# Kernel optimization log

Hardware: AMD Instinct MI355X
Metric: run time of the kernel (lower is better)

Reference implementation:

```python
import jax, jax.numpy as jnp
import numpy as np

HEADS = 8
DIM_HEAD = 64
SCALE = DIM_HEAD ** -0.5

def setup_inputs() -> dict:
    key = jax.random.key(0)
    ks = jax.random.split(key, 6)
    b, n, m, qd, cd = 4, 2048, 2048, 256, 256
    inner = HEADS * DIM_HEAD
    return {
        "x": jax.random.normal(ks[0], (b, n, qd), jnp.float32),
        "context": jax.random.normal(ks[1], (b, m, cd), jnp.float32),
        "Wq": jax.random.normal(ks[2], (inner, qd), jnp.float32) * 0.02,
        "bq": jnp.zeros((inner,), jnp.float32),
        "Wkv": jax.random.normal(ks[3], (2 * inner, cd), jnp.float32) * 0.02,
        "bkv": jnp.zeros((2 * inner,), jnp.float32),
        "Wo": jax.random.normal(ks[4], (qd, inner), jnp.float32) * 0.02,
        "bo": jnp.zeros((qd,), jnp.float32),
    }

def reference(x, context, Wq, bq, Wkv, bkv, Wo, bo):
    b, n, _ = x.shape
    m = context.shape[1]
    inner = HEADS * DIM_HEAD
    # 1x1 conv projections == pointwise linear
    q = jnp.einsum('bnd,ed->bne', x, Wq) + bq            # [b, n, inner]
    kv = jnp.einsum('bmd,ed->bme', context, Wkv) + bkv    # [b, m, 2*inner]
    k, v = kv[..., :inner], kv[..., inner:]
    q = q.reshape(b, n, HEADS, DIM_HEAD).transpose(0, 2, 1, 3)  # [b,h,n,d]
    k = k.reshape(b, m, HEADS, DIM_HEAD).transpose(0, 2, 1, 3)
    v = v.reshape(b, m, HEADS, DIM_HEAD).transpose(0, 2, 1, 3)
    sim = jnp.einsum('bhid,bhjd->bhij', q, k) * SCALE     # [b,h,n,m]
    attn = jax.nn.softmax(sim, axis=-1)
    out = jnp.einsum('bhij,bhjd->bhid', attn, v)          # [b,h,n,d]
    out = out.transpose(0, 2, 1, 3).reshape(b, n, inner)  # [b,n,inner]
    return jnp.einsum('bne,oe->bno', out, Wo) + bo        # [b,n,query_dim]
```

## Files before the change

kernel.cpp:

```cpp
#include <hip/hip_runtime.h>
#include <hip/hip_bf16.h>

#define NB 4
#define SEQ 2048
#define NHEADS 8

typedef __attribute__((ext_vector_type(8))) short bf16x8;
typedef __attribute__((ext_vector_type(4))) short bf16x4;
typedef __attribute__((ext_vector_type(4))) float f32x4;

__device__ inline short f2bf(float x) {
    union { float f; unsigned u; } v; v.f = x;
    unsigned r = v.u + 0x7FFF + ((v.u >> 16) & 1);
    return (short)(r >> 16);
}

__device__ inline unsigned pack2bf(float a, float b) {
    __hip_bfloat162 h = __float22bfloat162_rn(make_float2(a, b));
    unsigned u; __builtin_memcpy(&u, &h, 4);
    return u;
}

__device__ inline bf16x8 pack8(float4 a, float4 b) {
    union { unsigned u[4]; bf16x8 v; } r;
    r.u[0] = pack2bf(a.x, a.y);
    r.u[1] = pack2bf(a.z, a.w);
    r.u[2] = pack2bf(b.x, b.y);
    r.u[3] = pack2bf(b.z, b.w);
    return r.v;
}

__global__ __launch_bounds__(256) void cvt_xc(
    const float* __restrict__ x, const float* __restrict__ ctx,
    short* __restrict__ xb, short* __restrict__ cb)
{
    const int i = blockIdx.x * 256 + threadIdx.x;
    const float* src; short* dst; int off;
    if (i < 524288) { src = x;   dst = xb; off = i; }
    else            { src = ctx; dst = cb; off = i - 524288; }
    const float4 v = ((const float4*)src)[off];
    uint2 o2;
    o2.x = pack2bf(v.x, v.y);
    o2.y = pack2bf(v.z, v.w);
    *(uint2*)(dst + (size_t)off * 4) = o2;
}

template <bool CVT_A, bool CVT_W, bool OUT_BF16>
__global__ __launch_bounds__(256) void gemm128(
    const void* __restrict__ A_, const void* __restrict__ W_,
    const float* __restrict__ bias, void* __restrict__ out,
    int K, int Ccols, float scale)
{
    __shared__ short As[128 * 64];
    __shared__ short Ws[128 * 64];
    const int tid = threadIdx.x;
    const int w = tid >> 6, lane = tid & 63, low = lane & 15, quad = lane >> 4;
    const int wm = w >> 1, wn = w & 1;
    const int rM0 = blockIdx.y * 128, c0 = blockIdx.x * 128;
    const int srow = tid >> 3, sj = tid & 7;

    f32x4 acc[4][4];
#pragma unroll
    for (int mt = 0; mt < 4; ++mt)
#pragma unroll
        for (int nt = 0; nt < 4; ++nt) acc[mt][nt] = (f32x4){0.f, 0.f, 0.f, 0.f};

    float4 paf[4][2], pwf[4][2];
    bf16x8 pab[4], pwb[4];

    auto loadA = [&](int c, int k0) {
        const int row = c * 32 + srow;
        if constexpr (CVT_A) {
            const float* p = (const float*)A_ + (size_t)(rM0 + row) * K + k0 + sj * 8;
            paf[c][0] = ((const float4*)p)[0];
            paf[c][1] = ((const float4*)p)[1];
        } else {
            pab[c] = *(const bf16x8*)((const short*)A_ + (size_t)(rM0 + row) * K + k0 + sj * 8);
        }
    };
    auto loadW = [&](int c, int k0) {
        const int row = c * 32 + srow;
        if constexpr (CVT_W) {
            const float* p = (const float*)W_ + (size_t)(c0 + row) * K + k0 + sj * 8;
            pwf[c][0] = ((const float4*)p)[0];
            pwf[c][1] = ((const float4*)p)[1];
        } else {
            pwb[c] = *(const bf16x8*)((const short*)W_ + (size_t)(c0 + row) * K + k0 + sj * 8);
        }
    };

#pragma unroll
    for (int c = 0; c < 4; ++c) { loadA(c, 0); loadW(c, 0); }

    int k0 = 0;
    for (;;) {
        __syncthreads();
#pragma unroll
        for (int c = 0; c < 4; ++c) {
            const int row = c * 32 + srow;
            const int pc = sj ^ (row & 7);
            if constexpr (CVT_A) *(bf16x8*)(&As[row * 64 + pc * 8]) = pack8(paf[c][0], paf[c][1]);
            else                 *(bf16x8*)(&As[row * 64 + pc * 8]) = pab[c];
            if constexpr (CVT_W) *(bf16x8*)(&Ws[row * 64 + pc * 8]) = pack8(pwf[c][0], pwf[c][1]);
            else                 *(bf16x8*)(&Ws[row * 64 + pc * 8]) = pwb[c];
        }
        __syncthreads();
        const int kn = k0 + 64;
        if (kn < K) {
#pragma unroll
            for (int c = 0; c < 4; ++c) { loadA(c, kn); loadW(c, kn); }
        }
#pragma unroll
        for (int kh = 0; kh < 2; ++kh) {
            bf16x8 af[4], bfv[4];
#pragma unroll
            for (int t = 0; t < 4; ++t) {
                const int ra = wm * 64 + t * 16 + low;
                af[t] = *(const bf16x8*)(&As[ra * 64 + ((kh * 4 + quad) ^ (ra & 7)) * 8]);
                const int rb = wn * 64 + t * 16 + low;
                bfv[t] = *(const bf16x8*)(&Ws[rb * 64 + ((kh * 4 + quad) ^ (rb & 7)) * 8]);
            }
#pragma unroll
            for (int mt = 0; mt < 4; ++mt)
#pragma unroll
                for (int nt = 0; nt < 4; ++nt)
                    acc[mt][nt] = __builtin_amdgcn_mfma_f32_16x16x32_bf16(af[mt], bfv[nt], acc[mt][nt], 0, 0, 0);
        }
        k0 = kn;
        if (k0 >= K) break;
    }

#pragma unroll
    for (int nt = 0; nt < 4; ++nt) {
        const int col = c0 + wn * 64 + nt * 16 + low;
        const float bv = bias[col];
#pragma unroll
        for (int mt = 0; mt < 4; ++mt) {
            const size_t rbase = (size_t)(rM0 + wm * 64 + mt * 16 + quad * 4);
#pragma unroll
            for (int r = 0; r < 4; ++r) {
                const float val = (acc[mt][nt][r] + bv) * scale;
                if (OUT_BF16) ((short*)out)[(rbase + r) * Ccols + col] = f2bf(val);
                else          ((float*)out)[(rbase + r) * Ccols + col] = val;
            }
        }
    }
}

template <bool CVT_A, bool CVT_W, bool OUT_BF16>
__global__ __launch_bounds__(256) void gemm64(
    const void* __restrict__ A_, const void* __restrict__ W_,
    const float* __restrict__ bias, void* __restrict__ out,
    int K, int Ccols, float scale)
{
    __shared__ short As[64 * 64];
    __shared__ short Ws[64 * 64];
    const int tid = threadIdx.x;
    const int w = tid >> 6, lane = tid & 63, low = lane & 15, quad = lane >> 4;
    const int wm = w >> 1, wn = w & 1;
    const int r0 = blockIdx.y * 64, c0 = blockIdx.x * 64;
    const int srow = tid >> 2;
    const int sc = (tid & 3) * 2;

    f32x4 acc[2][2];
#pragma unroll
    for (int mt = 0; mt < 2; ++mt)
#pragma unroll
        for (int nt = 0; nt < 2; ++nt) acc[mt][nt] = (f32x4){0.f, 0.f, 0.f, 0.f};

    float4 paf[2][2], pwf[2][2];
    bf16x8 pab[2], pwb[2];

    auto loadA = [&](int k0) {
        if constexpr (CVT_A) {
            const float* p = (const float*)A_ + (size_t)(r0 + srow) * K + k0 + sc * 8;
            paf[0][0] = ((const float4*)p)[0]; paf[0][1] = ((const float4*)p)[1];
            paf[1][0] = ((const float4*)p)[2]; paf[1][1] = ((const float4*)p)[3];
        } else {
            const short* p = (const short*)A_ + (size_t)(r0 + srow) * K + k0 + sc * 8;
            pab[0] = ((const bf16x8*)p)[0];
            pab[1] = ((const bf16x8*)p)[1];
        }
    };
    auto loadW = [&](int k0) {
        if constexpr (CVT_W) {
            const float* p = (const float*)W_ + (size_t)(c0 + srow) * K + k0 + sc * 8;
            pwf[0][0] = ((const float4*)p)[0]; pwf[0][1] = ((const float4*)p)[1];
            pwf[1][0] = ((const float4*)p)[2]; pwf[1][1] = ((const float4*)p)[3];
        } else {
            const short* p = (const short*)W_ + (size_t)(c0 + srow) * K + k0 + sc * 8;
            pwb[0] = ((const bf16x8*)p)[0];
            pwb[1] = ((const bf16x8*)p)[1];
        }
    };

    loadA(0); loadW(0);

    int k0 = 0;
    for (;;) {
        __syncthreads();
#pragma unroll
        for (int c = 0; c < 2; ++c) {
            const int pc = (sc + c) ^ (srow & 7);
            if constexpr (CVT_A) *(bf16x8*)(&As[srow * 64 + pc * 8]) = pack8(paf[c][0], paf[c][1]);
            else                 *(bf16x8*)(&As[srow * 64 + pc * 8]) = pab[c];
            if constexpr (CVT_W) *(bf16x8*)(&Ws[srow * 64 + pc * 8]) = pack8(pwf[c][0], pwf[c][1]);
            else                 *(bf16x8*)(&Ws[srow * 64 + pc * 8]) = pwb[c];
        }
        __syncthreads();
        const int kn = k0 + 64;
        if (kn < K) { loadA(kn); loadW(kn); }
#pragma unroll
        for (int kh = 0; kh < 2; ++kh) {
            bf16x8 af[2], bfv[2];
#pragma unroll
            for (int t = 0; t < 2; ++t) {
                const int ra = wm * 32 + t * 16 + low;
                af[t] = *(const bf16x8*)(&As[ra * 64 + ((kh * 4 + quad) ^ (ra & 7)) * 8]);
                const int rb = wn * 32 + t * 16 + low;
                bfv[t] = *(const bf16x8*)(&Ws[rb * 64 + ((kh * 4 + quad) ^ (rb & 7)) * 8]);
            }
#pragma unroll
            for (int mt = 0; mt < 2; ++mt)
#pragma unroll
                for (int nt = 0; nt < 2; ++nt)
                    acc[mt][nt] = __builtin_amdgcn_mfma_f32_16x16x32_bf16(af[mt], bfv[nt], acc[mt][nt], 0, 0, 0);
        }
        k0 = kn;
        if (k0 >= K) break;
    }

#pragma unroll
    for (int nt = 0; nt < 2; ++nt) {
        const int col = c0 + wn * 32 + nt * 16 + low;
        const float bv = bias[col];
#pragma unroll
        for (int mt = 0; mt < 2; ++mt) {
            const size_t rbase = (size_t)(r0 + wm * 32 + mt * 16 + quad * 4);
#pragma unroll
            for (int r = 0; r < 4; ++r) {
                const float val = (acc[mt][nt][r] + bv) * scale;
                if (OUT_BF16) ((short*)out)[(rbase + r) * Ccols + col] = f2bf(val);
                else          ((float*)out)[(rbase + r) * Ccols + col] = val;
            }
        }
    }
}

#define KST 72
#define VST 72
#define PST 72

__global__ __launch_bounds__(256) void attn_mfma(
    const short* __restrict__ q2,
    const short* __restrict__ kv2,
    short* __restrict__ o)
{
    __shared__ short Ks[64 * KST];
    __shared__ short Vt[64 * VST];
    __shared__ short Ps[4][32 * PST];

    const int tid = threadIdx.x;
    const int w = tid >> 6;
    const int lane = tid & 63;
    const int low = lane & 15;
    const int quad = lane >> 4;

    const int flat = blockIdx.x;
    const int h = flat & 7;
    const int rest = flat >> 3;
    const int qtile = rest & 15;
    const int b = rest >> 4;
    const int iq0 = qtile * 128;

    bf16x8 qf[2][2];
#pragma unroll
    for (int qt = 0; qt < 2; ++qt)
#pragma unroll
        for (int kh = 0; kh < 2; ++kh)
            qf[qt][kh] = *(const bf16x8*)(q2 + (size_t)(b * SEQ + iq0 + w * 32 + qt * 16 + low) * 512
                                          + h * 64 + kh * 32 + quad * 8);

    const short* kbase = kv2 + (size_t)(b * SEQ) * 1024 + h * 64;
    const short* vbase = kbase + 512;
    short* pw = &Ps[w][0];

    float lsum[2] = {0.f, 0.f};
    f32x4 oacc[2][4];
#pragma unroll
    for (int qt = 0; qt < 2; ++qt)
#pragma unroll
        for (int dt = 0; dt < 4; ++dt) oacc[qt][dt] = (f32x4){0.f, 0.f, 0.f, 0.f};

    const int krow = tid >> 2;
    const int kc = (tid & 3) * 16;
    const int vk4 = (tid & 15) * 4;
    const int vd4 = (tid >> 4) * 4;

    bf16x8 pk0, pk1;
    bf16x4 pv0, pv1, pv2, pv3;
    {
        const short* ksrc = kbase + (size_t)krow * 1024 + kc;
        pk0 = *(const bf16x8*)(ksrc);
        pk1 = *(const bf16x8*)(ksrc + 8);
        const short* vs = vbase + (size_t)vk4 * 1024 + vd4;
        pv0 = *(const bf16x4*)(vs);
        pv1 = *(const bf16x4*)(vs + 1024);
        pv2 = *(const bf16x4*)(vs + 2048);
        pv3 = *(const bf16x4*)(vs + 3072);
    }

    for (int jt = 0; jt < SEQ / 64; ++jt) {
        __syncthreads();
        *(bf16x8*)(&Ks[krow * KST + kc]) = pk0;
        *(bf16x8*)(&Ks[krow * KST + kc + 8]) = pk1;
        {
            bf16x4 c0_, c1_, c2_, c3_;
            c0_[0] = pv0[0]; c0_[1] = pv1[0]; c0_[2] = pv2[0]; c0_[3] = pv3[0];
            c1_[0] = pv0[1]; c1_[1] = pv1[1]; c1_[2] = pv2[1]; c1_[3] = pv3[1];
            c2_[0] = pv0[2]; c2_[1] = pv1[2]; c2_[2] = pv2[2]; c2_[3] = pv3[2];
            c3_[0] = pv0[3]; c3_[1] = pv1[3]; c3_[2] = pv2[3]; c3_[3] = pv3[3];
            *(bf16x4*)(&Vt[(vd4 + 0) * VST + vk4]) = c0_;
            *(bf16x4*)(&Vt[(vd4 + 1) * VST + vk4]) = c1_;
            *(bf16x4*)(&Vt[(vd4 + 2) * VST + vk4]) = c2_;
            *(bf16x4*)(&Vt[(vd4 + 3) * VST + vk4]) = c3_;
        }
        __syncthreads();

        if (jt + 1 < SEQ / 64) {
            const short* ksrc = kbase + (size_t)((jt + 1) * 64 + krow) * 1024 + kc;
            pk0 = *(const bf16x8*)(ksrc);
            pk1 = *(const bf16x8*)(ksrc + 8);
            const short* vs = vbase + (size_t)((jt + 1) * 64 + vk4) * 1024 + vd4;
            pv0 = *(const bf16x4*)(vs);
            pv1 = *(const bf16x4*)(vs + 1024);
            pv2 = *(const bf16x4*)(vs + 2048);
            pv3 = *(const bf16x4*)(vs + 3072);
        }

#pragma unroll
        for (int nt = 0; nt < 4; ++nt) {
            const bf16x8 kf0 = *(const bf16x8*)(&Ks[(nt * 16 + low) * KST + quad * 8]);
            const bf16x8 kf1 = *(const bf16x8*)(&Ks[(nt * 16 + low) * KST + 32 + quad * 8]);
#pragma unroll
            for (int qt = 0; qt < 2; ++qt) {
                f32x4 s = (f32x4){0.f, 0.f, 0.f, 0.f};
                s = __builtin_amdgcn_mfma_f32_16x16x32_bf16(kf0, qf[qt][0], s, 0, 0, 0);
                s = __builtin_amdgcn_mfma_f32_16x16x32_bf16(kf1, qf[qt][1], s, 0, 0, 0);
                const float p0 = __builtin_amdgcn_exp2f(s[0]);
                const float p1 = __builtin_amdgcn_exp2f(s[1]);
                const float p2 = __builtin_amdgcn_exp2f(s[2]);
                const float p3 = __builtin_amdgcn_exp2f(s[3]);
                lsum[qt] += (p0 + p1) + (p2 + p3);
                uint2 u;
                u.x = pack2bf(p0, p1);
                u.y = pack2bf(p2, p3);
                *(uint2*)(&pw[(qt * 16 + low) * PST + nt * 16 + quad * 4]) = u;
            }
        }
        __builtin_amdgcn_wave_barrier();

#pragma unroll
        for (int kb = 0; kb < 2; ++kb) {
            bf16x8 pfr[2];
#pragma unroll
            for (int qt = 0; qt < 2; ++qt)
                pfr[qt] = *(const bf16x8*)(&pw[(qt * 16 + low) * PST + kb * 32 + quad * 8]);
#pragma unroll
            for (int dt = 0; dt < 4; ++dt) {
                const bf16x8 vf = *(const bf16x8*)(&Vt[(dt * 16 + low) * VST + kb * 32 + quad * 8]);
                oacc[0][dt] = __builtin_amdgcn_mfma_f32_16x16x32_bf16(pfr[0], vf, oacc[0][dt], 0, 0, 0);
                oacc[1][dt] = __builtin_amdgcn_mfma_f32_16x16x32_bf16(pfr[1], vf, oacc[1][dt], 0, 0, 0);
            }
        }
        __builtin_amdgcn_wave_barrier();
    }

#pragma unroll
    for (int qt = 0; qt < 2; ++qt) {
        float lv = lsum[qt];
        lv += __shfl_xor(lv, 16);
        lv += __shfl_xor(lv, 32);
        float linv[4];
#pragma unroll
        for (int r = 0; r < 4; ++r)
            linv[r] = 1.f / __shfl(lv, quad * 4 + r);
        short* obase = o + (size_t)(b * SEQ + iq0 + w * 32 + qt * 16 + quad * 4) * 512 + h * 64;
#pragma unroll
        for (int r = 0; r < 4; ++r)
#pragma unroll
            for (int dt = 0; dt < 4; ++dt)
                obase[(size_t)r * 512 + dt * 16 + low] = f2bf(oacc[qt][dt][r] * linv[r]);
    }
}

extern "C" void kernel_launch(void* const* d_in, const int* in_sizes, int n_in,
                              void* d_out, int out_size, void* d_ws, size_t ws_size,
                              hipStream_t stream) {
    const float* x   = (const float*)d_in[0];
    const float* ctx = (const float*)d_in[1];
    const float* Wq  = (const float*)d_in[2];
    const float* bq  = (const float*)d_in[3];
    const float* Wkv = (const float*)d_in[4];
    const float* bkv = (const float*)d_in[5];
    const float* Wo  = (const float*)d_in[6];
    const float* bo  = (const float*)d_in[7];
    float* out = (float*)d_out;

    const int ROWS = NB * SEQ;
    short* xb   = (short*)d_ws;
    short* cb   = xb + (size_t)ROWS * 256;
    short* q2b  = cb + (size_t)ROWS * 256;
    short* kv2b = q2b + (size_t)ROWS * 512;
    short* owsb = kv2b + (size_t)ROWS * 1024;

    const float qscale = 0.125f * 1.44269504088896f;

    cvt_xc<<<4096, 256, 0, stream>>>(x, ctx, xb, cb);

    gemm64<false, true, true><<<dim3(512 / 64, ROWS / 64), 256, 0, stream>>>(
        xb, Wq, bq, q2b, 256, 512, qscale);
    gemm128<false, true, true><<<dim3(1024 / 128, ROWS / 128), 256, 0, stream>>>(
        cb, Wkv, bkv, kv2b, 256, 1024, 1.0f);
    attn_mfma<<<NB * NHEADS * (SEQ / 128), 256, 0, stream>>>(q2b, kv2b, owsb);
    gemm64<false, true, false><<<dim3(256 / 64, ROWS / 64), 256, 0, stream>>>(
        owsb, Wo, bo, out, 512, 256, 1.0f);
}
```

Baseline: 172.2 us.

## Split attention over two KV halves and combine partials in output projection

Attention blocks are doubled, with each block handling half of the key/value sequence. Each block writes unnormalized bf16 numerators and per-row softmax sums to workspace. The output-projection GEMM then adds the two halves, divides by the combined sum while staging A into shared memory, and applies Wo. This is meant to raise parallelism and occupancy in the attention kernel, at the cost of extra workspace traffic. It also relies on the two halves sharing a softmax reference, since no per-half max rescaling is done.

```diff
diff --git a/kernel.cpp b/kernel.cpp
--- a/kernel.cpp
+++ b/kernel.cpp
@@ -4,6 +4,7 @@
 #define NB 4
 #define SEQ 2048
 #define NHEADS 8
+#define ROWS (NB * SEQ)
 
 typedef __attribute__((ext_vector_type(8))) short bf16x8;
 typedef __attribute__((ext_vector_type(4))) short bf16x4;
@@ -28,6 +29,13 @@
     r.u[2] = pack2bf(b.x, b.y);
     r.u[3] = pack2bf(b.z, b.w);
     return r.v;
+}
+
+__device__ inline unsigned comb2(unsigned w1, unsigned w2, float inv) {
+    union { unsigned v; float f; } a, b, c, d;
+    a.v = w1 << 16;          b.v = w2 << 16;
+    c.v = w1 & 0xffff0000u;  d.v = w2 & 0xffff0000u;
+    return pack2bf((a.f + b.f) * inv, (c.f + d.f) * inv);
 }
 
 __global__ __launch_bounds__(256) void cvt_xc(
@@ -45,10 +53,10 @@
     *(uint2*)(dst + (size_t)off * 4) = o2;
 }
 
-template <bool CVT_A, bool CVT_W, bool OUT_BF16>
+template <bool CVT_W>
 __global__ __launch_bounds__(256) void gemm128(
-    const void* __restrict__ A_, const void* __restrict__ W_,
-    const float* __restrict__ bias, void* __restrict__ out,
+    const short* __restrict__ A, const void* __restrict__ W_,
+    const float* __restrict__ bias, short* __restrict__ out,
     int K, int Ccols, float scale)
 {
     __shared__ short As[128 * 64];
@@ -65,18 +73,12 @@
 #pragma unroll
         for (int nt = 0; nt < 4; ++nt) acc[mt][nt] = (f32x4){0.f, 0.f, 0.f, 0.f};
 
-    float4 paf[4][2], pwf[4][2];
+    float4 pwf[4][2];
     bf16x8 pab[4], pwb[4];
 
     auto loadA = [&](int c, int k0) {
         const int row = c * 32 + srow;
-        if constexpr (CVT_A) {
-            const float* p = (const float*)A_ + (size_t)(rM0 + row) * K + k0 + sj * 8;
-            paf[c][0] = ((const float4*)p)[0];
-            paf[c][1] = ((const float4*)p)[1];
-        } else {
-            pab[c] = *(const bf16x8*)((const short*)A_ + (size_t)(rM0 + row) * K + k0 + sj * 8);
-        }
+        pab[c] = *(const bf16x8*)(A + (size_t)(rM0 + row) * K + k0 + sj * 8);
     };
     auto loadW = [&](int c, int k0) {
         const int row = c * 32 + srow;
@@ -99,8 +101,7 @@
         for (int c = 0; c < 4; ++c) {
             const int row = c * 32 + srow;
             const int pc = sj ^ (row & 7);
-            if constexpr (CVT_A) *(bf16x8*)(&As[row * 64 + pc * 8]) = pack8(paf[c][0], paf[c][1]);
-            else                 *(bf16x8*)(&As[row * 64 + pc * 8]) = pab[c];
+            *(bf16x8*)(&As[row * 64 + pc * 8]) = pab[c];
             if constexpr (CVT_W) *(bf16x8*)(&Ws[row * 64 + pc * 8]) = pack8(pwf[c][0], pwf[c][1]);
             else                 *(bf16x8*)(&Ws[row * 64 + pc * 8]) = pwb[c];
         }
@@ -138,19 +139,15 @@
         for (int mt = 0; mt < 4; ++mt) {
             const size_t rbase = (size_t)(rM0 + wm * 64 + mt * 16 + quad * 4);
 #pragma unroll
-            for (int r = 0; r < 4; ++r) {
-                const float val = (acc[mt][nt][r] + bv) * scale;
-                if (OUT_BF16) ((short*)out)[(rbase + r) * Ccols + col] = f2bf(val);
-                else          ((float*)out)[(rbase + r) * Ccols + col] = val;
-            }
-        }
-    }
-}
-
-template <bool CVT_A, bool CVT_W, bool OUT_BF16>
-__global__ __launch_bounds__(256) void gemm64(
-    const void* __restrict__ A_, const void* __restrict__ W_,
-    const float* __restrict__ bias, void* __restrict__ out,
+            for (int r = 0; r < 4; ++r)
+                out[(rbase + r) * Ccols + col] = f2bf((acc[mt][nt][r] + bv) * scale);
+        }
+    }
+}
+
+__global__ __launch_bounds__(256) void gemm64_q(
+    const short* __restrict__ A, const float* __restrict__ W,
+    const float* __restrict__ bias, short* __restrict__ out,
     int K, int Ccols, float scale)
 {
     __shared__ short As[64 * 64];
@@ -168,30 +165,18 @@
 #pragma unroll
         for (int nt = 0; nt < 2; ++nt) acc[mt][nt] = (f32x4){0.f, 0.f, 0.f, 0.f};
 
-    float4 paf[2][2], pwf[2][2];
-    bf16x8 pab[2], pwb[2];
+    bf16x8 pab[2];
+    float4 pwf[2][2];
 
     auto loadA = [&](int k0) {
-        if constexpr (CVT_A) {
-            const float* p = (const float*)A_ + (size_t)(r0 + srow) * K + k0 + sc * 8;
-            paf[0][0] = ((const float4*)p)[0]; paf[0][1] = ((const float4*)p)[1];
-            paf[1][0] = ((const float4*)p)[2]; paf[1][1] = ((const float4*)p)[3];
-        } else {
-            const short* p = (const short*)A_ + (size_t)(r0 + srow) * K + k0 + sc * 8;
-            pab[0] = ((const bf16x8*)p)[0];
-            pab[1] = ((const bf16x8*)p)[1];
-        }
+        const short* p = A + (size_t)(r0 + srow) * K + k0 + sc * 8;
+        pab[0] = ((const bf16x8*)p)[0];
+        pab[1] = ((const bf16x8*)p)[1];
     };
     auto loadW = [&](int k0) {
-        if constexpr (CVT_W) {
-            const float* p = (const float*)W_ + (size_t)(c0 + srow) * K + k0 + sc * 8;
-            pwf[0][0] = ((const float4*)p)[0]; pwf[0][1] = ((const float4*)p)[1];
-            pwf[1][0] = ((const float4*)p)[2]; pwf[1][1] = ((const float4*)p)[3];
-        } else {
-            const short* p = (const short*)W_ + (size_t)(c0 + srow) * K + k0 + sc * 8;
-            pwb[0] = ((const bf16x8*)p)[0];
-            pwb[1] = ((const bf16x8*)p)[1];
-        }
+        const float* p = W + (size_t)(c0 + srow) * K + k0 + sc * 8;
+        pwf[0][0] = ((const float4*)p)[0]; pwf[0][1] = ((const float4*)p)[1];
+        pwf[1][0] = ((const float4*)p)[2]; pwf[1][1] = ((const float4*)p)[3];
     };
 
     loadA(0); loadW(0);
@@ -202,10 +187,8 @@
 #pragma unroll
         for (int c = 0; c < 2; ++c) {
             const int pc = (sc + c) ^ (srow & 7);
-            if constexpr (CVT_A) *(bf16x8*)(&As[srow * 64 + pc * 8]) = pack8(paf[c][0], paf[c][1]);
-            else                 *(bf16x8*)(&As[srow * 64 + pc * 8]) = pab[c];
-            if constexpr (CVT_W) *(bf16x8*)(&Ws[srow * 64 + pc * 8]) = pack8(pwf[c][0], pwf[c][1]);
-            else                 *(bf16x8*)(&Ws[srow * 64 + pc * 8]) = pwb[c];
+            *(bf16x8*)(&As[srow * 64 + pc * 8]) = pab[c];
+            *(bf16x8*)(&Ws[srow * 64 + pc * 8]) = pack8(pwf[c][0], pwf[c][1]);
         }
         __syncthreads();
         const int kn = k0 + 64;
@@ -238,11 +221,108 @@
         for (int mt = 0; mt < 2; ++mt) {
             const size_t rbase = (size_t)(r0 + wm * 32 + mt * 16 + quad * 4);
 #pragma unroll
-            for (int r = 0; r < 4; ++r) {
-                const float val = (acc[mt][nt][r] + bv) * scale;
-                if (OUT_BF16) ((short*)out)[(rbase + r) * Ccols + col] = f2bf(val);
-                else          ((float*)out)[(rbase + r) * Ccols + col] = val;
+            for (int r = 0; r < 4; ++r)
+                out[(rbase + r) * Ccols + col] = f2bf((acc[mt][nt][r] + bv) * scale);
+        }
+    }
+}
+
+__global__ __launch_bounds__(256) void gemm64_ocomb(
+    const short* __restrict__ num, const float* __restrict__ lbuf,
+    const float* __restrict__ W, const float* __restrict__ bias,
+    float* __restrict__ out)
+{
+    const int K = 512, Ccols = 256;
+    const size_t NHALF = (size_t)ROWS * 512;
+    const int R8 = ROWS * 8;
+    __shared__ short As[64 * 64];
+    __shared__ short Ws[64 * 64];
+    const int tid = threadIdx.x;
+    const int w = tid >> 6, lane = tid & 63, low = lane & 15, quad = lane >> 4;
+    const int wm = w >> 1, wn = w & 1;
+    const int r0 = blockIdx.y * 64, c0 = blockIdx.x * 64;
+    const int srow = tid >> 2;
+    const int sc = (tid & 3) * 2;
+
+    f32x4 acc[2][2];
+#pragma unroll
+    for (int mt = 0; mt < 2; ++mt)
+#pragma unroll
+        for (int nt = 0; nt < 2; ++nt) acc[mt][nt] = (f32x4){0.f, 0.f, 0.f, 0.f};
+
+    uint4 pa1[2], pa2[2];
+    float pinv;
+    float4 pwf[2][2];
+
+    auto loadA = [&](int k0) {
+        const int hh = k0 >> 6;
+        const int row = r0 + srow;
+        pinv = lbuf[row * 8 + hh] + lbuf[R8 + row * 8 + hh];
+        const short* p1 = num + (size_t)row * 512 + k0 + sc * 8;
+        pa1[0] = ((const uint4*)p1)[0];
+        pa1[1] = ((const uint4*)p1)[1];
+        const short* p2 = p1 + NHALF;
+        pa2[0] = ((const uint4*)p2)[0];
+        pa2[1] = ((const uint4*)p2)[1];
+    };
+    auto loadW = [&](int k0) {
+        const float* p = W + (size_t)(c0 + srow) * K + k0 + sc * 8;
+        pwf[0][0] = ((const float4*)p)[0]; pwf[0][1] = ((const float4*)p)[1];
+        pwf[1][0] = ((const float4*)p)[2]; pwf[1][1] = ((const float4*)p)[3];
+    };
+
+    loadA(0); loadW(0);
+
+    int k0 = 0;
+    for (;;) {
+        __syncthreads();
+        {
+            const float inv = 1.f / pinv;
+#pragma unroll
+            for (int c = 0; c < 2; ++c) {
+                const int pc = (sc + c) ^ (srow & 7);
+                union { unsigned u[4]; bf16x8 v; } r;
+                r.u[0] = comb2(pa1[c].x, pa2[c].x, inv);
+                r.u[1] = comb2(pa1[c].y, pa2[c].y, inv);
+                r.u[2] = comb2(pa1[c].z, pa2[c].z, inv);
+                r.u[3] = comb2(pa1[c].w, pa2[c].w, inv);
+                *(bf16x8*)(&As[srow * 64 + pc * 8]) = r.v;
+                *(bf16x8*)(&Ws[srow * 64 + pc * 8]) = pack8(pwf[c][0], pwf[c][1]);
             }
+        }
+        __syncthreads();
+        const int kn = k0 + 64;
+        if (kn < K) { loadA(kn); loadW(kn); }
+#pragma unroll
+        for (int kh = 0; kh < 2; ++kh) {
+            bf16x8 af[2], bfv[2];
+#pragma unroll
+            for (int t = 0; t < 2; ++t) {
+                const int ra = wm * 32 + t * 16 + low;
+                af[t] = *(const bf16x8*)(&As[ra * 64 + ((kh * 4 + quad) ^ (ra & 7)) * 8]);
+                const int rb = wn * 32 + t * 16 + low;
+                bfv[t] = *(const bf16x8*)(&Ws[rb * 64 + ((kh * 4 + quad) ^ (rb & 7)) * 8]);
+            }
+#pragma unroll
+            for (int mt = 0; mt < 2; ++mt)
+#pragma unroll
+                for (int nt = 0; nt < 2; ++nt)
+                    acc[mt][nt] = __builtin_amdgcn_mfma_f32_16x16x32_bf16(af[mt], bfv[nt], acc[mt][nt], 0, 0, 0);
+        }
+        k0 = kn;
+        if (k0 >= K) break;
+    }
+
+#pragma unroll
+    for (int nt = 0; nt < 2; ++nt) {
+        const int col = c0 + wn * 32 + nt * 16 + low;
+        const float bv = bias[col];
+#pragma unroll
+        for (int mt = 0; mt < 2; ++mt) {
+            const size_t rbase = (size_t)(r0 + wm * 32 + mt * 16 + quad * 4);
+#pragma unroll
+            for (int r = 0; r < 4; ++r)
+                out[(rbase + r) * Ccols + col] = acc[mt][nt][r] + bv;
         }
     }
 }
@@ -254,7 +334,8 @@
 __global__ __launch_bounds__(256) void attn_mfma(
     const short* __restrict__ q2,
     const short* __restrict__ kv2,
-    short* __restrict__ o)
+    short* __restrict__ numb,
+    float* __restrict__ lbuf)
 {
     __shared__ short Ks[64 * KST];
     __shared__ short Vt[64 * VST];
@@ -269,9 +350,12 @@
     const int flat = blockIdx.x;
     const int h = flat & 7;
     const int rest = flat >> 3;
-    const int qtile = rest & 15;
-    const int b = rest >> 4;
+    const int half = rest & 1;
+    const int rest2 = rest >> 1;
+    const int qtile = rest2 & 15;
+    const int b = rest2 >> 4;
     const int iq0 = qtile * 128;
+    const int jt0 = half * 16;
 
     bf16x8 qf[2][2];
 #pragma unroll
@@ -300,17 +384,17 @@
     bf16x8 pk0, pk1;
     bf16x4 pv0, pv1, pv2, pv3;
     {
-        const short* ksrc = kbase + (size_t)krow * 1024 + kc;
+        const short* ksrc = kbase + (size_t)(jt0 * 64 + krow) * 1024 + kc;
         pk0 = *(const bf16x8*)(ksrc);
         pk1 = *(const bf16x8*)(ksrc + 8);
-        const short* vs = vbase + (size_t)vk4 * 1024 + vd4;
+        const short* vs = vbase + (size_t)(jt0 * 64 + vk4) * 1024 + vd4;
         pv0 = *(const bf16x4*)(vs);
         pv1 = *(const bf16x4*)(vs + 1024);
         pv2 = *(const bf16x4*)(vs + 2048);
         pv3 = *(const bf16x4*)(vs + 3072);
     }
 
-    for (int jt = 0; jt < SEQ / 64; ++jt) {
+    for (int jt = jt0; jt < jt0 + 16; ++jt) {
         __syncthreads();
         *(bf16x8*)(&Ks[krow * KST + kc]) = pk0;
         *(bf16x8*)(&Ks[krow * KST + kc + 8]) = pk1;
@@ -327,7 +411,7 @@
         }
         __syncthreads();
 
-        if (jt + 1 < SEQ / 64) {
+        if (jt + 1 < jt0 + 16) {
             const short* ksrc = kbase + (size_t)((jt + 1) * 64 + krow) * 1024 + kc;
             pk0 = *(const bf16x8*)(ksrc);
             pk1 = *(const bf16x8*)(ksrc + 8);
@@ -376,21 +460,21 @@
         __builtin_amdgcn_wave_barrier();
     }
 
+    short* nb = numb + (size_t)half * ROWS * 512;
+    float* lb = lbuf + (size_t)half * ROWS * 8;
 #pragma unroll
     for (int qt = 0; qt < 2; ++qt) {
         float lv = lsum[qt];
         lv += __shfl_xor(lv, 16);
         lv += __shfl_xor(lv, 32);
-        float linv[4];
+        if (quad == 0)
+            lb[(size_t)(b * SEQ + iq0 + w * 32 + qt * 16 + low) * 8 + h] = lv;
+        short* obase = nb + (size_t)(b * SEQ + iq0 + w * 32 + qt * 16 + quad * 4) * 512 + h * 64;
 #pragma unroll
         for (int r = 0; r < 4; ++r)
-            linv[r] = 1.f / __shfl(lv, quad * 4 + r);
-        short* obase = o + (size_t)(b * SEQ + iq0 + w * 32 + qt * 16 + quad * 4) * 512 + h * 64;
-#pragma unroll
-        for (int r = 0; r < 4; ++r)
 #pragma unroll
             for (int dt = 0; dt < 4; ++dt)
-                obase[(size_t)r * 512 + dt * 16 + low] = f2bf(oacc[qt][dt][r] * linv[r]);
+                obase[(size_t)r * 512 + dt * 16 + low] = f2bf(oacc[qt][dt][r]);
     }
 }
 
@@ -407,22 +491,23 @@
     const float* bo  = (const float*)d_in[7];
     float* out = (float*)d_out;
 
-    const int ROWS = NB * SEQ;
     short* xb   = (short*)d_ws;
     short* cb   = xb + (size_t)ROWS * 256;
     short* q2b  = cb + (size_t)ROWS * 256;
     short* kv2b = q2b + (size_t)ROWS * 512;
-    short* owsb = kv2b + (size_t)ROWS * 1024;
+    short* numb = kv2b + (size_t)ROWS * 1024;
+    float* lbuf = (float*)(numb + (size_t)2 * ROWS * 512);
 
     const float qscale = 0.125f * 1.44269504088896f;
 
     cvt_xc<<<4096, 256, 0, stream>>>(x, ctx, xb, cb);
 
-    gemm64<false, true, true><<<dim3(512 / 64, ROWS / 64), 256, 0, stream>>>(
+    gemm64_q<<<dim3(512 / 64, ROWS / 64), 256, 0, stream>>>(
         xb, Wq, bq, q2b, 256, 512, qscale);
-    gemm128<false, true, true><<<dim3(1024 / 128, ROWS / 128), 256, 0, stream>>>(
+    gemm128<true><<<dim3(1024 / 128, ROWS / 128), 256, 0, stream>>>(
         cb, Wkv, bkv, kv2b, 256, 1024, 1.0f);
-    attn_mfma<<<NB * NHEADS * (SEQ / 128), 256, 0, stream>>>(q2b, kv2b, owsb);
-    gemm64<false, true, false><<<dim3(256 / 64, ROWS / 64), 256, 0, stream>>>(
-        owsb, Wo, bo, out, 512, 256, 1.0f);
-}
+    attn_mfma<<<NB * NHEADS * (SEQ / 128) * 2, 256, 0, stream>>>(
+        q2b, kv2b, numb, lbuf);
+    gemm64_ocomb<<<dim3(256 / 64, ROWS / 64), 256, 0, stream>>>(
+        numb, lbuf, Wo, bo, out);
+}
```

New measurement: 172.4 us. About the same (+0.1%).
